# Kernel optimization log

Measured on AMD Instinct MI355X. Metric: run time of the kernel, lower is better.

The kernel has to match this reference:

```python
import jax, jax.numpy as jnp
import numpy as np

N_NODES = 50000
N_EDGES = 800000
IN_CH = 256
HID = 256
NUM_GRAPHS = 512
LEAKY_SLOPE = 0.01
EPS = 1e-5


def gcn_conv(x, src, dst, W, b):
    # src/dst already include self loops. Symmetric normalization D^-1/2 A_hat D^-1/2.
    deg = jnp.zeros((N_NODES,), x.dtype).at[dst].add(1.0)
    dinv = jax.lax.rsqrt(deg)  # deg >= 1 because of self loops
    norm = dinv[src] * dinv[dst]  # [E+N]
    h = x @ W  # [N, H] dense GEMM
    agg = jnp.zeros((N_NODES, W.shape[1]), x.dtype).at[dst].add(h[src] * norm[:, None])
    return agg + b


def layer_norm(x, w, b):
    mu = jnp.mean(x, axis=-1, keepdims=True)
    var = jnp.mean(jnp.square(x - mu), axis=-1, keepdims=True)
    return (x - mu) * jax.lax.rsqrt(var + EPS) * w + b


def setup_inputs() -> dict:
    key = jax.random.key(0)
    ks = jax.random.split(key, 8)
    x = jax.random.normal(ks[0], (N_NODES, IN_CH), dtype=jnp.float32)
    edge_index = jax.random.randint(ks[1], (2, N_EDGES), 0, N_NODES, dtype=jnp.int64)
    batch = jnp.sort(jax.random.randint(ks[2], (N_NODES,), 0, NUM_GRAPHS, dtype=jnp.int64))
    s1 = (2.0 / IN_CH) ** 0.5
    s2 = (2.0 / HID) ** 0.5
    W1 = jax.random.normal(ks[3], (IN_CH, HID), dtype=jnp.float32) * s1
    b1 = jnp.zeros((HID,), jnp.float32)
    W2 = jax.random.normal(ks[4], (HID, HID), dtype=jnp.float32) * s2
    b2 = jnp.zeros((HID,), jnp.float32)
    ln1_w = jnp.ones((HID,), jnp.float32)
    ln1_b = jnp.zeros((HID,), jnp.float32)
    ln2_w = jnp.ones((HID,), jnp.float32)
    ln2_b = jnp.zeros((HID,), jnp.float32)
    return {"x": x, "edge_index": edge_index, "batch": batch,
            "W1": W1, "b1": b1, "ln1_w": ln1_w, "ln1_b": ln1_b,
            "W2": W2, "b2": b2, "ln2_w": ln2_w, "ln2_b": ln2_b}


def reference(x, edge_index, batch, W1, b1, ln1_w, ln1_b, W2, b2, ln2_w, ln2_b):
    loop = jnp.arange(N_NODES, dtype=edge_index.dtype)
    src = jnp.concatenate([edge_index[0], loop])
    dst = jnp.concatenate([edge_index[1], loop])

    h = gcn_conv(x, src, dst, W1, b1)
    h = layer_norm(h, ln1_w, ln1_b)
    h = jnp.where(h >= 0, h, LEAKY_SLOPE * h)

    h = gcn_conv(h, src, dst, W2, b2)
    h = layer_norm(h, ln2_w, ln2_b)
    h = jnp.where(h >= 0, h, LEAKY_SLOPE * h)

    # global mean pool per graph (dropout is inference no-op)
    sums = jax.ops.segment_sum(h, batch, num_segments=NUM_GRAPHS)
    cnts = jax.ops.segment_sum(jnp.ones((N_NODES,), h.dtype), batch, num_segments=NUM_GRAPHS)
    return sums / jnp.maximum(cnts, 1.0)[:, None]
```

## Files before the change

kernel.cpp:

```cpp
#include <hip/hip_runtime.h>

#define N_NODES 50000
#define N_EDGES 800000
#define CH 256
#define NUM_GRAPHS 512
#define LEAKY 0.01f
#define LN_EPS 1e-5f
#define NBLK ((N_NODES + 255) / 256)

typedef __attribute__((ext_vector_type(4))) float f32x4;
typedef __attribute__((ext_vector_type(2))) float f32x2;
typedef __attribute__((ext_vector_type(8))) short bf16x8;

__device__ __forceinline__ float b2f(unsigned short u) {
    union { unsigned int i; float f; } x; x.i = ((unsigned int)u) << 16; return x.f;
}
__device__ __forceinline__ unsigned short f2b(float f) {
    union { float f; unsigned int i; } x; x.f = f;
    unsigned int r = x.i + 0x7fffu + ((x.i >> 16) & 1u);
    return (unsigned short)(r >> 16);
}
__device__ __forceinline__ f32x2 b2f2(unsigned int u) {
    union { unsigned int i; float f; } lo, hi;
    lo.i = u << 16; hi.i = u & 0xffff0000u;
    f32x2 r; r.x = lo.f; r.y = hi.f; return r;
}
__device__ __forceinline__ unsigned int pack2(float a, float b) {
    return (unsigned int)f2b(a) | ((unsigned int)f2b(b) << 16);
}
__device__ __forceinline__ void gload16(const void* g, void* l) {
    __builtin_amdgcn_global_load_lds((const __attribute__((address_space(1))) unsigned int*)g,
                                     (__attribute__((address_space(3))) unsigned int*)l, 16, 0, 0);
}

__global__ void prep(int* __restrict__ cnt,
                     const float* __restrict__ W1f, const float* __restrict__ W2f,
                     unsigned short* __restrict__ WT1, unsigned short* __restrict__ WT2) {
    int b = blockIdx.x;
    if (b < NBLK) {
        int i = b * 256 + threadIdx.x;
        if (i < N_NODES) cnt[i] = 0;
    } else {
        int bb = b - NBLK;
        int k = bb & 255;
        const float* W = (bb >> 8) ? W2f : W1f;
        unsigned short* WT = (bb >> 8) ? WT2 : WT1;
        WT[threadIdx.x * CH + k] = f2b(W[k * CH + threadIdx.x]);
    }
}

__global__ void count_deg(const int* __restrict__ dst, int* __restrict__ cnt) {
    int e = blockIdx.x * blockDim.x + threadIdx.x;
    if (e < N_EDGES) atomicAdd(&cnt[dst[e]], 1);
}

__global__ __launch_bounds__(256) void block_reduce(const int* __restrict__ cnt,
                                                    int* __restrict__ bsum,
                                                    float* __restrict__ dinv) {
    __shared__ int s[256];
    int tid = threadIdx.x;
    int i = blockIdx.x * 256 + tid;
    int v = (i < N_NODES) ? cnt[i] : 0;
    if (i < N_NODES) dinv[i] = rsqrtf(1.0f + (float)v);
    s[tid] = v;
    __syncthreads();
    #pragma unroll
    for (int off = 128; off > 0; off >>= 1) {
        if (tid < off) s[tid] += s[tid + off];
        __syncthreads();
    }
    if (tid == 0) bsum[blockIdx.x] = s[0];
}

__global__ __launch_bounds__(256) void block_scan(const int* __restrict__ cnt,
                                                  const int* __restrict__ bsum,
                                                  int* __restrict__ rowptr,
                                                  int* __restrict__ cursor) {
    __shared__ int s[256], sb[256];
    int tid = threadIdx.x;
    int i = blockIdx.x * 256 + tid;
    int bv = (tid < NBLK) ? bsum[tid] : 0;
    sb[tid] = bv;
    __syncthreads();
    #pragma unroll
    for (int off = 1; off < 256; off <<= 1) {
        int t = (tid >= off) ? sb[tid - off] : 0;
        __syncthreads();
        sb[tid] += t;
        __syncthreads();
    }
    const int base = (blockIdx.x == 0) ? 0 : sb[blockIdx.x - 1];
    int v = (i < N_NODES) ? cnt[i] : 0;
    s[tid] = v;
    __syncthreads();
    #pragma unroll
    for (int off = 1; off < 256; off <<= 1) {
        int t = (tid >= off) ? s[tid - off] : 0;
        __syncthreads();
        s[tid] += t;
        __syncthreads();
    }
    if (i < N_NODES) {
        int val = base + s[tid] - v;
        rowptr[i] = val;
        cursor[i] = val;
        if (i == N_NODES - 1) rowptr[N_NODES] = base + s[tid];
    }
}

__global__ void fill_csr(const int* __restrict__ src, const int* __restrict__ dst,
                         int* __restrict__ cursor, int* __restrict__ col) {
    int e = blockIdx.x * blockDim.x + threadIdx.x;
    if (e < N_EDGES) {
        int d = dst[e];
        int p = atomicAdd(&cursor[d], 1);
        col[p] = src[e];
    }
}

#define BM 128
#define BN 256
#define BK 64
#define SWZ(row, kb) (((row) * 128 + (kb) * 16) ^ (((row) & 7) << 4))

__global__ __launch_bounds__(256) void gemm_bf16(const unsigned short* __restrict__ A,
                                                 const unsigned short* __restrict__ BT,
                                                 const float* __restrict__ dinv,
                                                 unsigned short* __restrict__ out) {
    __shared__ unsigned short As[BM * BK];
    __shared__ unsigned short Bs[BN * BK];
    const int row0 = blockIdx.x * BM;
    const int tid = threadIdx.x;
    const int w = tid >> 6, l = tid & 63;
    const int wr = w >> 1, wc = w & 1;
    const int lr = l & 15, lg = l >> 4;
    const int sr = l >> 3, kbp = l & 7;

    f32x4 acc[4][8] = {};

    for (int k0 = 0; k0 < CH; k0 += BK) {
        #pragma unroll
        for (int it = 0; it < 4; it++) {
            const int R = (w * 4 + it) * 8;
            const int r = R + sr;
            const int kb = kbp ^ (r & 7);
            gload16(&A[(size_t)(row0 + r) * CH + k0 + kb * 8], (char*)As + R * 128);
        }
        #pragma unroll
        for (int it = 0; it < 8; it++) {
            const int R = w * 64 + it * 8;
            const int r = R + sr;
            const int kb = kbp ^ (r & 7);
            gload16(&BT[(size_t)r * CH + k0 + kb * 8], (char*)Bs + R * 128);
        }
        __syncthreads();
        #pragma unroll
        for (int ks = 0; ks < 2; ks++) {
            bf16x8 af[4], bfr[8];
            #pragma unroll
            for (int fm = 0; fm < 4; fm++) {
                int r = wr * 64 + fm * 16 + lr;
                af[fm] = *(const bf16x8*)((const char*)As + SWZ(r, ks * 4 + lg));
            }
            #pragma unroll
            for (int fn = 0; fn < 8; fn++) {
                int r = wc * 128 + fn * 16 + lr;
                bfr[fn] = *(const bf16x8*)((const char*)Bs + SWZ(r, ks * 4 + lg));
            }
            #pragma unroll
            for (int fm = 0; fm < 4; fm++)
                #pragma unroll
                for (int fn = 0; fn < 8; fn++)
                    acc[fm][fn] = __builtin_amdgcn_mfma_f32_16x16x32_bf16(af[fm], bfr[fn], acc[fm][fn], 0, 0, 0);
        }
        __syncthreads();
    }
    #pragma unroll
    for (int fm = 0; fm < 4; fm++) {
        #pragma unroll
        for (int r = 0; r < 4; r++) {
            int grow = row0 + wr * 64 + fm * 16 + lg * 4 + r;
            if (grow < N_NODES) {
                float s = dinv[grow];
                #pragma unroll
                for (int fn = 0; fn < 8; fn++) {
                    int gcol = wc * 128 + fn * 16 + lr;
                    out[(size_t)grow * CH + gcol] = f2b(acc[fm][fn][r] * s);
                }
            }
        }
    }
}

__global__ __launch_bounds__(256) void gemm_f32a(const float* __restrict__ Af,
                                                 const unsigned short* __restrict__ BT,
                                                 const float* __restrict__ dinv,
                                                 unsigned short* __restrict__ out) {
    __shared__ unsigned short As[BM * BK];
    __shared__ unsigned short Bs[BN * BK];
    const int row0 = blockIdx.x * BM;
    const int tid = threadIdx.x;
    const int w = tid >> 6, l = tid & 63;
    const int wr = w >> 1, wc = w & 1;
    const int lr = l & 15, lg = l >> 4;
    const int sr = l >> 3, kbp = l & 7;

    f32x4 acc[4][8] = {};

    for (int k0 = 0; k0 < CH; k0 += BK) {
        #pragma unroll
        for (int it = 0; it < 8; it++) {
            const int R = w * 64 + it * 8;
            const int r = R + sr;
            const int kb = kbp ^ (r & 7);
            gload16(&BT[(size_t)r * CH + k0 + kb * 8], (char*)Bs + R * 128);
        }
        #pragma unroll
        for (int it = 0; it < 4; it++) {
            int cidx = it * 256 + tid;
            int r = cidx >> 3, kb = cidx & 7;
            int grow = row0 + r;
            uint4 ua = make_uint4(0u, 0u, 0u, 0u);
            if (grow < N_NODES) {
                const float* ap = &Af[(size_t)grow * CH + k0 + kb * 8];
                float4 v0 = *(const float4*)ap;
                float4 v1 = *(const float4*)(ap + 4);
                ua = make_uint4(pack2(v0.x, v0.y), pack2(v0.z, v0.w),
                                pack2(v1.x, v1.y), pack2(v1.z, v1.w));
            }
            *(uint4*)((char*)As + SWZ(r, kb)) = ua;
        }
        __syncthreads();
        #pragma unroll
        for (int ks = 0; ks < 2; ks++) {
            bf16x8 af[4], bfr[8];
            #pragma unroll
            for (int fm = 0; fm < 4; fm++) {
                int r = wr * 64 + fm * 16 + lr;
                af[fm] = *(const bf16x8*)((const char*)As + SWZ(r, ks * 4 + lg));
            }
            #pragma unroll
            for (int fn = 0; fn < 8; fn++) {
                int r = wc * 128 + fn * 16 + lr;
                bfr[fn] = *(const bf16x8*)((const char*)Bs + SWZ(r, ks * 4 + lg));
            }
            #pragma unroll
            for (int fm = 0; fm < 4; fm++)
                #pragma unroll
                for (int fn = 0; fn < 8; fn++)
                    acc[fm][fn] = __builtin_amdgcn_mfma_f32_16x16x32_bf16(af[fm], bfr[fn], acc[fm][fn], 0, 0, 0);
        }
        __syncthreads();
    }
    #pragma unroll
    for (int fm = 0; fm < 4; fm++) {
        #pragma unroll
        for (int r = 0; r < 4; r++) {
            int grow = row0 + wr * 64 + fm * 16 + lg * 4 + r;
            if (grow < N_NODES) {
                float s = dinv[grow];
                #pragma unroll
                for (int fn = 0; fn < 8; fn++) {
                    int gcol = wc * 128 + fn * 16 + lr;
                    out[(size_t)grow * CH + gcol] = f2b(acc[fm][fn][r] * s);
                }
            }
        }
    }
}

__global__ __launch_bounds__(256) void agg_ln_bf16(const unsigned short* __restrict__ h,
                                                   const int* __restrict__ rowptr,
                                                   const int* __restrict__ col,
                                                   const float* __restrict__ dinv,
                                                   const float* __restrict__ bias,
                                                   const float* __restrict__ lnw,
                                                   const float* __restrict__ lnb,
                                                   unsigned short* __restrict__ out) {
    const int w = threadIdx.x >> 6, lane = threadIdx.x & 63;
    const int d = blockIdx.x * 4 + w;
    if (d >= N_NODES) return;
    const int c4 = lane * 4;
    const uint2* __restrict__ h2 = (const uint2*)h;

    f32x2 acc01, acc23;
    {
        uint2 u = h2[(unsigned)(d * 64 + lane)];
        acc01 = b2f2(u.x); acc23 = b2f2(u.y);
    }

    const int e0 = rowptr[d], e1 = rowptr[d + 1];
    for (int base = e0; base < e1; base += 64) {
        int nch = e1 - base; if (nch > 64) nch = 64;
        int cidx = (lane < nch) ? col[base + lane] : 0;
        int j = 0;
        for (; j + 8 <= nch; j += 8) {
            int s0 = __shfl(cidx, j),     s1 = __shfl(cidx, j + 1);
            int s2 = __shfl(cidx, j + 2), s3 = __shfl(cidx, j + 3);
            int s4 = __shfl(cidx, j + 4), s5 = __shfl(cidx, j + 5);
            int s6 = __shfl(cidx, j + 6), s7 = __shfl(cidx, j + 7);
            uint2 u0 = h2[(unsigned)(s0 * 64 + lane)];
            uint2 u1 = h2[(unsigned)(s1 * 64 + lane)];
            uint2 u2 = h2[(unsigned)(s2 * 64 + lane)];
            uint2 u3 = h2[(unsigned)(s3 * 64 + lane)];
            uint2 u4 = h2[(unsigned)(s4 * 64 + lane)];
            uint2 u5 = h2[(unsigned)(s5 * 64 + lane)];
            uint2 u6 = h2[(unsigned)(s6 * 64 + lane)];
            uint2 u7 = h2[(unsigned)(s7 * 64 + lane)];
            acc01 += b2f2(u0.x) + b2f2(u1.x) + b2f2(u2.x) + b2f2(u3.x);
            acc23 += b2f2(u0.y) + b2f2(u1.y) + b2f2(u2.y) + b2f2(u3.y);
            acc01 += b2f2(u4.x) + b2f2(u5.x) + b2f2(u6.x) + b2f2(u7.x);
            acc23 += b2f2(u4.y) + b2f2(u5.y) + b2f2(u6.y) + b2f2(u7.y);
        }
        for (; j + 4 <= nch; j += 4) {
            int s0 = __shfl(cidx, j),     s1 = __shfl(cidx, j + 1);
            int s2 = __shfl(cidx, j + 2), s3 = __shfl(cidx, j + 3);
            uint2 u0 = h2[(unsigned)(s0 * 64 + lane)];
            uint2 u1 = h2[(unsigned)(s1 * 64 + lane)];
            uint2 u2 = h2[(unsigned)(s2 * 64 + lane)];
            uint2 u3 = h2[(unsigned)(s3 * 64 + lane)];
            acc01 += b2f2(u0.x) + b2f2(u1.x) + b2f2(u2.x) + b2f2(u3.x);
            acc23 += b2f2(u0.y) + b2f2(u1.y) + b2f2(u2.y) + b2f2(u3.y);
        }
        for (; j < nch; j++) {
            int s = __shfl(cidx, j);
            uint2 u = h2[(unsigned)(s * 64 + lane)];
            acc01 += b2f2(u.x); acc23 += b2f2(u.y);
        }
    }
    float a0 = acc01.x, a1 = acc01.y, a2 = acc23.x, a3 = acc23.y;
    const float di = dinv[d];
    float4 bb = *(const float4*)&bias[c4];
    a0 = a0 * di + bb.x; a1 = a1 * di + bb.y; a2 = a2 * di + bb.z; a3 = a3 * di + bb.w;

    float s1 = a0 + a1 + a2 + a3;
    float s2 = a0 * a0 + a1 * a1 + a2 * a2 + a3 * a3;
    #pragma unroll
    for (int off = 32; off > 0; off >>= 1) {
        s1 += __shfl_xor(s1, off);
        s2 += __shfl_xor(s2, off);
    }
    const float mu = s1 * (1.0f / CH);
    const float rstd = rsqrtf(s2 * (1.0f / CH) - mu * mu + LN_EPS);
    float4 wv = *(const float4*)&lnw[c4];
    float4 bv = *(const float4*)&lnb[c4];
    float y0 = (a0 - mu) * rstd * wv.x + bv.x;
    float y1 = (a1 - mu) * rstd * wv.y + bv.y;
    float y2 = (a2 - mu) * rstd * wv.z + bv.z;
    float y3 = (a3 - mu) * rstd * wv.w + bv.w;
    y0 = fmaxf(y0, LEAKY * y0);
    y1 = fmaxf(y1, LEAKY * y1);
    y2 = fmaxf(y2, LEAKY * y2);
    y3 = fmaxf(y3, LEAKY * y3);
    *(ushort4*)&out[(size_t)d * CH + c4] = make_ushort4(f2b(y0), f2b(y1), f2b(y2), f2b(y3));
}

__global__ __launch_bounds__(256) void pool_mean_bf16(const unsigned short* __restrict__ feat,
                                                      const int* __restrict__ batch,
                                                      float* __restrict__ out) {
    const int g = blockIdx.x;
    const int w = threadIdx.x >> 6, lane = threadIdx.x & 63;
    int lo = 0, hi = N_NODES;
    while (lo < hi) { int mid = (lo + hi) >> 1; if (batch[mid] < g) lo = mid + 1; else hi = mid; }
    const int start = lo;
    hi = N_NODES;
    while (lo < hi) { int mid = (lo + hi) >> 1; if (batch[mid] < g + 1) lo = mid + 1; else hi = mid; }
    const int end = lo;

    float a0 = 0.f, a1 = 0.f, a2 = 0.f, a3 = 0.f;
    for (int n = start + w; n < end; n += 4) {
        ushort4 u = *(const ushort4*)&feat[(size_t)n * CH + lane * 4];
        a0 += b2f(u.x); a1 += b2f(u.y); a2 += b2f(u.z); a3 += b2f(u.w);
    }
    __shared__ float4 red[4][64];
    red[w][lane] = make_float4(a0, a1, a2, a3);
    __syncthreads();
    if (w == 0) {
        float4 t0 = red[0][lane], t1 = red[1][lane], t2 = red[2][lane], t3 = red[3][lane];
        const float inv = (end > start) ? 1.0f / (float)(end - start) : 0.0f;
        float4 o = make_float4((t0.x + t1.x + t2.x + t3.x) * inv,
                               (t0.y + t1.y + t2.y + t3.y) * inv,
                               (t0.z + t1.z + t2.z + t3.z) * inv,
                               (t0.w + t1.w + t2.w + t3.w) * inv);
        *(float4*)&out[(size_t)g * CH + lane * 4] = o;
    }
}

static inline size_t align256(size_t x) { return (x + 255) & ~(size_t)255; }

extern "C" void kernel_launch(void* const* d_in, const int* in_sizes, int n_in,
                              void* d_out, int out_size, void* d_ws, size_t ws_size,
                              hipStream_t stream) {
    const float* x    = (const float*)d_in[0];
    const int*   edge = (const int*)d_in[1];
    const int*   batch= (const int*)d_in[2];
    const float* W1   = (const float*)d_in[3];
    const float* b1   = (const float*)d_in[4];
    const float* ln1w = (const float*)d_in[5];
    const float* ln1b = (const float*)d_in[6];
    const float* W2   = (const float*)d_in[7];
    const float* b2   = (const float*)d_in[8];
    const float* ln2w = (const float*)d_in[9];
    const float* ln2b = (const float*)d_in[10];

    const int* src = edge;
    const int* dst = edge + N_EDGES;

    char* p = (char*)d_ws;
    int* cnt    = (int*)p;  p += align256(N_NODES * 4);
    int* cursor = (int*)p;  p += align256(N_NODES * 4);
    int* rowptr = (int*)p;  p += align256((N_NODES + 1) * 4);
    int* bsum   = (int*)p;  p += align256(NBLK * 4);
    float* dinv = (float*)p; p += align256(N_NODES * 4);
    int* col    = (int*)p;  p += align256(N_EDGES * 4);
    unsigned short* wt1 = (unsigned short*)p; p += align256(CH * CH * 2);
    unsigned short* wt2 = (unsigned short*)p; p += align256(CH * CH * 2);
    unsigned short* bufA = (unsigned short*)p; p += align256((size_t)N_NODES * CH * 2);
    unsigned short* bufB = (unsigned short*)p; p += align256((size_t)N_NODES * CH * 2);
    p += 32768;

    prep<<<NBLK + 2 * CH, 256, 0, stream>>>(cnt, W1, W2, wt1, wt2);
    count_deg<<<(N_EDGES + 255) / 256, 256, 0, stream>>>(dst, cnt);
    block_reduce<<<NBLK, 256, 0, stream>>>(cnt, bsum, dinv);
    block_scan<<<NBLK, 256, 0, stream>>>(cnt, bsum, rowptr, cursor);
    fill_csr<<<(N_EDGES + 255) / 256, 256, 0, stream>>>(src, dst, cursor, col);

    const int ggrid = (N_NODES + BM - 1) / BM;
    gemm_f32a<<<ggrid, 256, 0, stream>>>(x, wt1, dinv, bufA);
    agg_ln_bf16<<<(N_NODES + 3) / 4, 256, 0, stream>>>(bufA, rowptr, col, dinv, b1, ln1w, ln1b, bufB);
    gemm_bf16<<<ggrid, 256, 0, stream>>>(bufB, wt2, dinv, bufA);
    agg_ln_bf16<<<(N_NODES + 3) / 4, 256, 0, stream>>>(bufA, rowptr, col, dinv, b2, ln2w, ln2b, bufB);
    pool_mean_bf16<<<NUM_GRAPHS, 256, 0, stream>>>(bufB, batch, (float*)d_out);
}
```

Baseline: 296.9 us.

## Restructure GEMMs: stage full-K A tile in LDS, split N across grid, read B from global

Both GEMM kernels now load the whole 128x256 A row-block into shared memory once with a single barrier, instead of looping over K in 64-wide chunks with two barriers per step. The output columns are split across a second grid dimension, so each block computes a 128x128 tile. B fragments are read directly from global memory (the small weight matrix stays cache-resident) rather than being staged in LDS. This doubles the grid and removes the K-loop synchronisation, but A is loaded twice (once per column half), the blocks use 64KB of LDS, which may limit occupancy, and B reads go uncoalesced through the cache.

```diff
diff --git a/kernel.cpp b/kernel.cpp
--- a/kernel.cpp
+++ b/kernel.cpp
@@ -119,62 +119,52 @@
 }
 
 #define BM 128
-#define BN 256
-#define BK 64
-#define SWZ(row, kb) (((row) * 128 + (kb) * 16) ^ (((row) & 7) << 4))
+#define SWZ2(r, c16) (((r) * 512 + (c16) * 16) ^ (((r) & 7) << 4))
 
 __global__ __launch_bounds__(256) void gemm_bf16(const unsigned short* __restrict__ A,
                                                  const unsigned short* __restrict__ BT,
                                                  const float* __restrict__ dinv,
                                                  unsigned short* __restrict__ out) {
-    __shared__ unsigned short As[BM * BK];
-    __shared__ unsigned short Bs[BN * BK];
+    __shared__ unsigned short As[BM * CH];
     const int row0 = blockIdx.x * BM;
+    const int col0 = blockIdx.y * 128;
     const int tid = threadIdx.x;
     const int w = tid >> 6, l = tid & 63;
     const int wr = w >> 1, wc = w & 1;
     const int lr = l & 15, lg = l >> 4;
-    const int sr = l >> 3, kbp = l & 7;
-
-    f32x4 acc[4][8] = {};
-
-    for (int k0 = 0; k0 < CH; k0 += BK) {
-        #pragma unroll
-        for (int it = 0; it < 4; it++) {
-            const int R = (w * 4 + it) * 8;
-            const int r = R + sr;
-            const int kb = kbp ^ (r & 7);
-            gload16(&A[(size_t)(row0 + r) * CH + k0 + kb * 8], (char*)As + R * 128);
-        }
-        #pragma unroll
-        for (int it = 0; it < 8; it++) {
-            const int R = w * 64 + it * 8;
-            const int r = R + sr;
-            const int kb = kbp ^ (r & 7);
-            gload16(&BT[(size_t)r * CH + k0 + kb * 8], (char*)Bs + R * 128);
-        }
-        __syncthreads();
-        #pragma unroll
-        for (int ks = 0; ks < 2; ks++) {
-            bf16x8 af[4], bfr[8];
+
+    {
+        const int es = l >> 5, c16 = l & 31;
+        #pragma unroll
+        for (int it = 0; it < 16; it++) {
+            const int r = it * 8 + w * 2 + es;
+            const int kb = c16 ^ (r & 7);
+            gload16(&A[(size_t)(row0 + r) * CH + kb * 8],
+                    (char*)As + (it * 8 + w * 2) * 512);
+        }
+    }
+    __syncthreads();
+
+    f32x4 acc[4][4] = {};
+    #pragma unroll
+    for (int ks = 0; ks < 8; ks++) {
+        bf16x8 af[4], bfr[4];
+        #pragma unroll
+        for (int fm = 0; fm < 4; fm++) {
+            int r = wr * 64 + fm * 16 + lr;
+            af[fm] = *(const bf16x8*)((const char*)As + SWZ2(r, ks * 4 + lg));
+        }
+        #pragma unroll
+        for (int fn = 0; fn < 4; fn++) {
+            bfr[fn] = *(const bf16x8*)&BT[(size_t)(col0 + wc * 64 + fn * 16 + lr) * CH + ks * 32 + lg * 8];
+        }
+        #pragma unroll
+        for (int fm = 0; fm < 4; fm++)
             #pragma unroll
-            for (int fm = 0; fm < 4; fm++) {
-                int r = wr * 64 + fm * 16 + lr;
-                af[fm] = *(const bf16x8*)((const char*)As + SWZ(r, ks * 4 + lg));
-            }
-            #pragma unroll
-            for (int fn = 0; fn < 8; fn++) {
-                int r = wc * 128 + fn * 16 + lr;
-                bfr[fn] = *(const bf16x8*)((const char*)Bs + SWZ(r, ks * 4 + lg));
-            }
-            #pragma unroll
-            for (int fm = 0; fm < 4; fm++)
-                #pragma unroll
-                for (int fn = 0; fn < 8; fn++)
-                    acc[fm][fn] = __builtin_amdgcn_mfma_f32_16x16x32_bf16(af[fm], bfr[fn], acc[fm][fn], 0, 0, 0);
-        }
-        __syncthreads();
-    }
+            for (int fn = 0; fn < 4; fn++)
+                acc[fm][fn] = __builtin_amdgcn_mfma_f32_16x16x32_bf16(af[fm], bfr[fn], acc[fm][fn], 0, 0, 0);
+    }
+
     #pragma unroll
     for (int fm = 0; fm < 4; fm++) {
         #pragma unroll
@@ -183,8 +173,8 @@
             if (grow < N_NODES) {
                 float s = dinv[grow];
                 #pragma unroll
-                for (int fn = 0; fn < 8; fn++) {
-                    int gcol = wc * 128 + fn * 16 + lr;
+                for (int fn = 0; fn < 4; fn++) {
+                    int gcol = col0 + wc * 64 + fn * 16 + lr;
                     out[(size_t)grow * CH + gcol] = f2b(acc[fm][fn][r] * s);
                 }
             }
@@ -196,62 +186,51 @@
                                                  const unsigned short* __restrict__ BT,
                                                  const float* __restrict__ dinv,
                                                  unsigned short* __restrict__ out) {
-    __shared__ unsigned short As[BM * BK];
-    __shared__ unsigned short Bs[BN * BK];
+    __shared__ unsigned short As[BM * CH];
     const int row0 = blockIdx.x * BM;
+    const int col0 = blockIdx.y * 128;
     const int tid = threadIdx.x;
     const int w = tid >> 6, l = tid & 63;
     const int wr = w >> 1, wc = w & 1;
     const int lr = l & 15, lg = l >> 4;
-    const int sr = l >> 3, kbp = l & 7;
-
-    f32x4 acc[4][8] = {};
-
-    for (int k0 = 0; k0 < CH; k0 += BK) {
-        #pragma unroll
-        for (int it = 0; it < 8; it++) {
-            const int R = w * 64 + it * 8;
-            const int r = R + sr;
-            const int kb = kbp ^ (r & 7);
-            gload16(&BT[(size_t)r * CH + k0 + kb * 8], (char*)Bs + R * 128);
-        }
-        #pragma unroll
-        for (int it = 0; it < 4; it++) {
-            int cidx = it * 256 + tid;
-            int r = cidx >> 3, kb = cidx & 7;
-            int grow = row0 + r;
-            uint4 ua = make_uint4(0u, 0u, 0u, 0u);
-            if (grow < N_NODES) {
-                const float* ap = &Af[(size_t)grow * CH + k0 + kb * 8];
-                float4 v0 = *(const float4*)ap;
-                float4 v1 = *(const float4*)(ap + 4);
-                ua = make_uint4(pack2(v0.x, v0.y), pack2(v0.z, v0.w),
-                                pack2(v1.x, v1.y), pack2(v1.z, v1.w));
-            }
-            *(uint4*)((char*)As + SWZ(r, kb)) = ua;
-        }
-        __syncthreads();
-        #pragma unroll
-        for (int ks = 0; ks < 2; ks++) {
-            bf16x8 af[4], bfr[8];
+
+    #pragma unroll
+    for (int it = 0; it < 16; it++) {
+        int cidx = it * 256 + tid;
+        int r = cidx >> 5, kb = cidx & 31;
+        int grow = row0 + r;
+        uint4 ua = make_uint4(0u, 0u, 0u, 0u);
+        if (grow < N_NODES) {
+            const float* ap = &Af[(size_t)grow * CH + kb * 8];
+            float4 v0 = *(const float4*)ap;
+            float4 v1 = *(const float4*)(ap + 4);
+            ua = make_uint4(pack2(v0.x, v0.y), pack2(v0.z, v0.w),
+                            pack2(v1.x, v1.y), pack2(v1.z, v1.w));
+        }
+        *(uint4*)((char*)As + SWZ2(r, kb)) = ua;
+    }
+    __syncthreads();
+
+    f32x4 acc[4][4] = {};
+    #pragma unroll
+    for (int ks = 0; ks < 8; ks++) {
+        bf16x8 af[4], bfr[4];
+        #pragma unroll
+        for (int fm = 0; fm < 4; fm++) {
+            int r = wr * 64 + fm * 16 + lr;
+            af[fm] = *(const bf16x8*)((const char*)As + SWZ2(r, ks * 4 + lg));
+        }
+        #pragma unroll
+        for (int fn = 0; fn < 4; fn++) {
+            bfr[fn] = *(const bf16x8*)&BT[(size_t)(col0 + wc * 64 + fn * 16 + lr) * CH + ks * 32 + lg * 8];
+        }
+        #pragma unroll
+        for (int fm = 0; fm < 4; fm++)
             #pragma unroll
-            for (int fm = 0; fm < 4; fm++) {
-                int r = wr * 64 + fm * 16 + lr;
-                af[fm] = *(const bf16x8*)((const char*)As + SWZ(r, ks * 4 + lg));
-            }
-            #pragma unroll
-            for (int fn = 0; fn < 8; fn++) {
-                int r = wc * 128 + fn * 16 + lr;
-                bfr[fn] = *(const bf16x8*)((const char*)Bs + SWZ(r, ks * 4 + lg));
-            }
-            #pragma unroll
-            for (int fm = 0; fm < 4; fm++)
-                #pragma unroll
-                for (int fn = 0; fn < 8; fn++)
-                    acc[fm][fn] = __builtin_amdgcn_mfma_f32_16x16x32_bf16(af[fm], bfr[fn], acc[fm][fn], 0, 0, 0);
-        }
-        __syncthreads();
-    }
+            for (int fn = 0; fn < 4; fn++)
+                acc[fm][fn] = __builtin_amdgcn_mfma_f32_16x16x32_bf16(af[fm], bfr[fn], acc[fm][fn], 0, 0, 0);
+    }
+
     #pragma unroll
     for (int fm = 0; fm < 4; fm++) {
         #pragma unroll
@@ -260,8 +239,8 @@
             if (grow < N_NODES) {
                 float s = dinv[grow];
                 #pragma unroll
-                for (int fn = 0; fn < 8; fn++) {
-                    int gcol = wc * 128 + fn * 16 + lr;
+                for (int fn = 0; fn < 4; fn++) {
+                    int gcol = col0 + wc * 64 + fn * 16 + lr;
                     out[(size_t)grow * CH + gcol] = f2b(acc[fm][fn][r] * s);
                 }
             }
@@ -417,7 +396,7 @@
     unsigned short* wt2 = (unsigned short*)p; p += align256(CH * CH * 2);
     unsigned short* bufA = (unsigned short*)p; p += align256((size_t)N_NODES * CH * 2);
     unsigned short* bufB = (unsigned short*)p; p += align256((size_t)N_NODES * CH * 2);
-    p += 32768;
+    p += 65536;
 
     prep<<<NBLK + 2 * CH, 256, 0, stream>>>(cnt, W1, W2, wt1, wt2);
     count_deg<<<(N_EDGES + 255) / 256, 256, 0, stream>>>(dst, cnt);
@@ -425,7 +404,7 @@
     block_scan<<<NBLK, 256, 0, stream>>>(cnt, bsum, rowptr, cursor);
     fill_csr<<<(N_EDGES + 255) / 256, 256, 0, stream>>>(src, dst, cursor, col);
 
-    const int ggrid = (N_NODES + BM - 1) / BM;
+    dim3 ggrid((N_NODES + BM - 1) / BM, 2);
     gemm_f32a<<<ggrid, 256, 0, stream>>>(x, wt1, dinv, bufA);
     agg_ln_bf16<<<(N_NODES + 3) / 4, 256, 0, stream>>>(bufA, rowptr, col, dinv, b1, ln1w, ln1b, bufB);
     gemm_bf16<<<ggrid, 256, 0, stream>>>(bufB, wt2, dinv, bufA);
```

After: 304.9 us. +2.7%, slower.
